# Optimization experiments

Measured on AMD Instinct MI355X. Metric: run time of the kernel, lower is better.

The kernel has to match this reference:

```python
import jax, jax.numpy as jnp
import numpy as np

WS = (7, 7)  # window size
NUM_HEADS = 16


def _relative_position_index(ws):
    # Deterministic int index table, computed exactly as in the torch module.
    coords = np.stack(np.meshgrid(np.arange(ws[0]), np.arange(ws[1]), indexing='ij'))  # [2,Wh,Ww]
    coords = coords.reshape(2, -1)                       # [2, N]
    rel = coords[:, :, None] - coords[:, None, :]        # [2, N, N]
    rel = rel.transpose(1, 2, 0)                         # [N, N, 2]
    rel = rel + np.array([ws[0] - 1, ws[1] - 1])
    rel[:, :, 0] *= 2 * ws[1] - 1
    return jnp.asarray(rel.sum(-1), dtype=jnp.int32)     # [N, N]


def setup_inputs() -> dict:
    key = jax.random.key(0)
    ks = jax.random.split(key, 5)
    B_, N, C = 2048, WS[0] * WS[1], 512
    nw = 64
    return {
        'x': jax.random.normal(ks[0], (B_, N, C), dtype=jnp.float32),
        'mask': jax.random.normal(ks[1], (nw, N, N), dtype=jnp.float32),
        'qkv_w': jax.random.normal(ks[2], (3 * C, C), dtype=jnp.float32) * 0.02,
        'qkv_b': jax.random.normal(ks[3], (3 * C,), dtype=jnp.float32) * 0.02,
        'rpb_table': jax.random.normal(ks[4], ((2 * WS[0] - 1) * (2 * WS[1] - 1), NUM_HEADS), dtype=jnp.float32) * 0.02,
    }


def reference(x, mask, qkv_w, qkv_b, rpb_table):
    B_, N, C = x.shape
    H = NUM_HEADS
    hd = C // H
    scale = hd ** -0.5

    # qkv projection: [B_, N, 3, H, hd] -> q, k, v each [B_, H, N, hd]
    qkv = (jnp.einsum('bnc,oc->bno', x, qkv_w) + qkv_b)
    qkv = qkv.reshape(B_, N, 3, H, hd).transpose(2, 0, 3, 1, 4)
    q, k, v = qkv[0], qkv[1], qkv[2]

    attn = jnp.einsum('bhnd,bhmd->bhnm', q * scale, k)  # [B_, H, N, N]

    rel_idx = _relative_position_index(WS)                       # [N, N]
    bias = rpb_table[rel_idx.reshape(-1)].reshape(N, N, H)       # gather
    attn = attn + bias.transpose(2, 0, 1)[None]                  # [1, H, N, N]

    nw = mask.shape[0]
    attn = attn.reshape(B_ // nw, nw, H, N, N) + mask[None, :, None]
    attn = attn.reshape(B_, H, N, N)
    attn = jax.nn.softmax(attn, axis=-1)

    out = jnp.einsum('bhnm,bhmd->bhnd', attn, v)
    out = out.transpose(0, 2, 1, 3).reshape(B_, N, C)
    # NOTE: source assigns `X = self.proj(x)` but returns `x`, so the
    # output projection is dead code; we faithfully return pre-proj output.
    return out
```

## Files before the change

kernel.cpp:

```cpp
#include <hip/hip_runtime.h>
#include <cstdint>
#include <cstddef>

typedef __bf16 bf16x8 __attribute__((ext_vector_type(8)));
typedef float f32x4 __attribute__((ext_vector_type(4)));
typedef unsigned short u16x8 __attribute__((ext_vector_type(8)));

#define VT_LD 56
#define LDE 144

__device__ __forceinline__ unsigned short f2bf(float f) {
  unsigned int u = __builtin_bit_cast(unsigned int, f);
  u += 0x7FFFu + ((u >> 16) & 1u);
  return (unsigned short)(u >> 16);
}

__device__ __forceinline__ void gload_lds16(const void* g, void* l) {
  __builtin_amdgcn_global_load_lds((const __attribute__((address_space(1))) void*)g,
                                   (__attribute__((address_space(3))) void*)l, 16, 0, 0);
}

__global__ void conv_f2b_k(const float* __restrict__ src, unsigned short* __restrict__ dst, long n8) {
  long i = (long)blockIdx.x * blockDim.x + threadIdx.x;
  long stride = (long)gridDim.x * blockDim.x;
  for (; i < n8; i += stride) {
    float4 a = *(const float4*)(src + i * 8);
    float4 b = *(const float4*)(src + i * 8 + 4);
    u16x8 p;
    p[0]=f2bf(a.x); p[1]=f2bf(a.y); p[2]=f2bf(a.z); p[3]=f2bf(a.w);
    p[4]=f2bf(b.x); p[5]=f2bf(b.y); p[6]=f2bf(b.z); p[7]=f2bf(b.w);
    *(u16x8*)(dst + i * 8) = p;
  }
}

__global__ void build_bias_k(const float* __restrict__ rpb, float* __restrict__ biasT) {
  int idx = blockIdx.x * 256 + threadIdx.x;
  if (idx >= 16 * 2401) return;
  int h = idx / 2401;
  int rem = idx - h * 2401;
  int i = rem / 49, j = rem - (rem / 49) * 49;
  int r1 = i / 7, c1 = i - r1 * 7;
  int r2 = j / 7, c2 = j - r2 * 7;
  int ri = (r1 - r2 + 6) * 13 + (c1 - c2 + 6);
  biasT[idx] = rpb[ri * 16 + h];
}

__global__ __launch_bounds__(256, 3) void qkv_gemm_k(
    const unsigned short* __restrict__ xb, const float* __restrict__ qkv_b,
    const unsigned short* __restrict__ wb,
    unsigned short* __restrict__ qs, unsigned short* __restrict__ kk,
    unsigned short* __restrict__ vt)
{
  __shared__ __align__(16) unsigned short smem[18432];
  unsigned short* Ab = smem;
  unsigned short* Bb = smem + 8192;

  int bid = blockIdx.x;
  int sw = (bid & 7) * 1176 + (bid >> 3);
  int mt = sw / 12, nt = sw - mt * 12;
  long m0 = (long)mt * 128;
  int  n0 = nt * 128;
  int  s  = n0 >> 9;

  int t = threadIdx.x;
  int lane = t & 63, wv = t >> 6;
  int g = lane >> 4, q = lane & 15;
  int wrow = wv >> 1, wcol = wv & 1;

  f32x4 acc[4][4] = {};

  int schunk = (t & 3) ^ ((t >> 3) & 3);
  const unsigned short* ag0 = xb + (m0 + (t >> 2)) * 512 + schunk * 8;
  const unsigned short* ag1 = ag0 + 64 * 512;
  const unsigned short* bg0 = wb + (size_t)(n0 + (t >> 2)) * 512 + schunk * 8;
  const unsigned short* bg1 = bg0 + 64 * 512;
  unsigned short* alA  = Ab + wv * 512;
  unsigned short* alA2 = Ab + 2048 + wv * 512;
  unsigned short* blB  = Bb + wv * 512;
  unsigned short* blB2 = Bb + 2048 + wv * 512;

  int roff = (8 * g) ^ (((q >> 1) & 3) << 3);
  const unsigned short* arb = Ab + (wrow * 64 + q) * 32 + roff;
  const unsigned short* brb = Bb + (wcol * 64 + q) * 32 + roff;

#define STAGE(KT, BOFF) do {                    \
    int kof = (KT) * 32;                        \
    gload_lds16(ag0 + kof, alA  + (BOFF));      \
    gload_lds16(ag1 + kof, alA2 + (BOFF));      \
    gload_lds16(bg0 + kof, blB  + (BOFF));      \
    gload_lds16(bg1 + kof, blB2 + (BOFF));      \
  } while (0)

#define COMPUTE(BOFF) do {                                                     \
    bf16x8 af[4], bfr[4];                                                      \
    _Pragma("unroll")                                                          \
    for (int i2 = 0; i2 < 4; ++i2) af[i2]  = *(const bf16x8*)(arb + (BOFF) + i2 * 512); \
    _Pragma("unroll")                                                          \
    for (int j2 = 0; j2 < 4; ++j2) bfr[j2] = *(const bf16x8*)(brb + (BOFF) + j2 * 512); \
    _Pragma("unroll")                                                          \
    for (int i2 = 0; i2 < 4; ++i2)                                             \
      _Pragma("unroll")                                                        \
      for (int j2 = 0; j2 < 4; ++j2)                                           \
        acc[i2][j2] = __builtin_amdgcn_mfma_f32_16x16x32_bf16(af[i2], bfr[j2], acc[i2][j2], 0, 0, 0); \
  } while (0)

  STAGE(0, 0);
  __syncthreads();
  for (int kt = 0; kt < 16; kt += 2) {
    STAGE(kt + 1, 4096);
    COMPUTE(0);
    __syncthreads();
    if (kt + 2 < 16) STAGE(kt + 2, 0);
    COMPUTE(4096);
    __syncthreads();
  }
#undef STAGE
#undef COMPUTE

  int   nl[4];
  float bias[4];
  #pragma unroll
  for (int j2 = 0; j2 < 4; ++j2) {
    nl[j2] = wcol * 64 + j2 * 16 + q;
    bias[j2] = qkv_b[n0 + nl[j2]];
  }

  if (s < 2) {
    float sc = (s == 0) ? 0.17677669529663687f : 1.0f;
    #pragma unroll
    for (int i2 = 0; i2 < 4; ++i2) {
      #pragma unroll
      for (int r = 0; r < 4; ++r) {
        int ml = wrow * 64 + i2 * 16 + 4 * g + r;
        #pragma unroll
        for (int j2 = 0; j2 < 4; ++j2)
          smem[ml * LDE + nl[j2]] = f2bf((acc[i2][j2][r] + bias[j2]) * sc);
      }
    }
    __syncthreads();
    unsigned short* dst = (s == 0) ? qs : kk;
    int c8 = (t & 15) * 8;
    int d0 = c8 & 31;
    int h  = ((n0 + c8) >> 5) & 15;
    #pragma unroll
    for (int p = 0; p < 8; ++p) {
      int row = p * 16 + (t >> 4);
      unsigned int gm = (unsigned int)m0 + row;
      unsigned int b  = gm / 49;
      unsigned int i  = gm - b * 49;
      u16x8 val = *(const u16x8*)(smem + row * LDE + c8);
      *(u16x8*)(dst + ((size_t)(b * 16 + h) * 49 + i) * 32 + d0) = val;
    }
  } else {
    #pragma unroll
    for (int j2 = 0; j2 < 4; ++j2) {
      int d = nl[j2] & 31;
      int h = ((n0 + nl[j2]) >> 5) & 15;
      #pragma unroll
      for (int i2 = 0; i2 < 4; ++i2) {
        unsigned int gm0 = (unsigned int)m0 + wrow * 64 + i2 * 16 + 4 * g;
        unsigned int b0 = gm0 / 49;
        unsigned int i0 = gm0 - b0 * 49;
        unsigned short hv[4];
        #pragma unroll
        for (int r = 0; r < 4; ++r) hv[r] = f2bf(acc[i2][j2][r] + bias[j2]);
        if (i0 <= 45) {
          unsigned short* base = vt + ((size_t)(b0 * 16 + h) * 32 + d) * VT_LD;
          if ((i0 & 1) == 0) {
            *(unsigned int*)(base + i0)     = (unsigned int)hv[0] | ((unsigned int)hv[1] << 16);
            *(unsigned int*)(base + i0 + 2) = (unsigned int)hv[2] | ((unsigned int)hv[3] << 16);
          } else {
            base[i0] = hv[0];
            *(unsigned int*)(base + i0 + 1) = (unsigned int)hv[1] | ((unsigned int)hv[2] << 16);
            base[i0 + 3] = hv[3];
          }
        } else {
          #pragma unroll
          for (int r = 0; r < 4; ++r) {
            unsigned int gm = gm0 + r;
            unsigned int b = gm / 49;
            unsigned int i = gm - b * 49;
            vt[((size_t)(b * 16 + h) * 32 + d) * VT_LD + i] = hv[r];
          }
        }
      }
    }
  }
}

__global__ __launch_bounds__(256, 2) void win_attn_k(
    const unsigned short* __restrict__ qs, const unsigned short* __restrict__ kk,
    const unsigned short* __restrict__ vt, const float* __restrict__ biasT,
    const float* __restrict__ mask, float* __restrict__ out)
{
  __shared__ float mlds[49 * 49];
  __shared__ unsigned short plds[4][64 * 72];

  int b = blockIdx.x;
  int t = threadIdx.x;
  int lane = t & 63, wv = t >> 6;
  int g = lane >> 4, q = lane & 15;

  const float* msrc = mask + (size_t)(b & 63) * 2401;
  for (int idx = t; idx < 2401; idx += 256) mlds[idx] = msrc[idx];
  __syncthreads();

  unsigned short* pl = plds[wv];

  for (int hh = 0; hh < 4; ++hh) {
    int h = wv * 4 + hh;
    const unsigned short* qh = qs + (size_t)(b * 16 + h) * (49 * 32);
    const unsigned short* kh = kk + (size_t)(b * 16 + h) * (49 * 32);
    const unsigned short* vh = vt + (size_t)(b * 16 + h) * (32 * VT_LD);
    const float* bhp = biasT + h * 2401;

    bf16x8 aq[4], bk[4];
    #pragma unroll
    for (int it = 0; it < 4; ++it) {
      int row = it * 16 + q; row = row > 48 ? 48 : row;
      aq[it] = *(const bf16x8*)(qh + row * 32 + 8 * g);
    }
    #pragma unroll
    for (int jt = 0; jt < 4; ++jt) {
      int row = jt * 16 + q; row = row > 48 ? 48 : row;
      bk[jt] = *(const bf16x8*)(kh + row * 32 + 8 * g);
    }
    f32x4 zero = {0.f, 0.f, 0.f, 0.f};
    f32x4 st[4][4];
    __builtin_amdgcn_s_setprio(1);
    #pragma unroll
    for (int it = 0; it < 4; ++it)
      #pragma unroll
      for (int jt = 0; jt < 4; ++jt)
        st[it][jt] = __builtin_amdgcn_mfma_f32_16x16x32_bf16(aq[it], bk[jt], zero, 0, 0, 0);
    __builtin_amdgcn_s_setprio(0);

    float rinv[4][4];
    #pragma unroll
    for (int it = 0; it < 4; ++it) {
      #pragma unroll
      for (int r = 0; r < 4; ++r) {
        int i = it * 16 + 4 * g + r;
        int ic = i > 48 ? 48 : i;
        float vj[4];
        #pragma unroll
        for (int jt = 0; jt < 4; ++jt) {
          int j = jt * 16 + q;
          float val;
          if (j < 49) val = st[it][jt][r] + bhp[ic * 49 + j] + mlds[ic * 49 + j];
          else        val = -__builtin_inff();
          vj[jt] = val;
        }
        float mx = fmaxf(fmaxf(vj[0], vj[1]), fmaxf(vj[2], vj[3]));
        #pragma unroll
        for (int off = 1; off < 16; off <<= 1) mx = fmaxf(mx, __shfl_xor(mx, off));
        float sm = 0.f;
        #pragma unroll
        for (int jt = 0; jt < 4; ++jt) {
          float p = __expf(vj[jt] - mx);
          st[it][jt][r] = p;
          sm += p;
        }
        #pragma unroll
        for (int off = 1; off < 16; off <<= 1) sm += __shfl_xor(sm, off);
        rinv[it][r] = 1.0f / sm;
      }
    }

    #pragma unroll
    for (int it = 0; it < 4; ++it)
      #pragma unroll
      for (int jt = 0; jt < 4; ++jt)
        #pragma unroll
        for (int r = 0; r < 4; ++r) {
          int i = it * 16 + 4 * g + r;
          int j = jt * 16 + q;
          pl[i * 72 + j] = f2bf(st[it][jt][r]);
        }

    f32x4 oacc[4][2] = {};
    #pragma unroll
    for (int ktt = 0; ktt < 2; ++ktt) {
      bf16x8 pa[4], bv[2];
      #pragma unroll
      for (int it = 0; it < 4; ++it)
        pa[it] = *(const bf16x8*)(pl + (it * 16 + q) * 72 + ktt * 32 + 8 * g);
      #pragma unroll
      for (int dt = 0; dt < 2; ++dt)
        bv[dt] = *(const bf16x8*)(vh + (dt * 16 + q) * VT_LD + ktt * 32 + 8 * g);
      __builtin_amdgcn_s_setprio(1);
      #pragma unroll
      for (int it = 0; it < 4; ++it)
        #pragma unroll
        for (int dt = 0; dt < 2; ++dt)
          oacc[it][dt] = __builtin_amdgcn_mfma_f32_16x16x32_bf16(pa[it], bv[dt], oacc[it][dt], 0, 0, 0);
      __builtin_amdgcn_s_setprio(0);
    }

    #pragma unroll
    for (int it = 0; it < 4; ++it) {
      #pragma unroll
      for (int dt = 0; dt < 2; ++dt) {
        #pragma unroll
        for (int r = 0; r < 4; ++r) {
          int i = it * 16 + 4 * g + r;
          if (i < 49) {
            int d = dt * 16 + q;
            out[(size_t)(b * 49 + i) * 512 + h * 32 + d] = oacc[it][dt][r] * rinv[it][r];
          }
        }
      }
    }
  }
}

extern "C" void kernel_launch(void* const* d_in, const int* in_sizes, int n_in,
                              void* d_out, int out_size, void* d_ws, size_t ws_size,
                              hipStream_t stream) {
  const float* x     = (const float*)d_in[0];
  const float* mask  = (const float*)d_in[1];
  const float* qkv_w = (const float*)d_in[2];
  const float* qkv_b = (const float*)d_in[3];
  const float* rpb   = (const float*)d_in[4];
  float* out = (float*)d_out;

  const size_t QS_OFF   = 0;
  const size_t KK_OFF   = 102760448;
  const size_t VT_OFF   = 205520896;
  const size_t BIAS_OFF = 322961408;
  const size_t WB_OFF   = 323115072;
  const size_t NEED     = 324687936;
  if (ws_size < NEED) return;

  char* ws = (char*)d_ws;
  unsigned short* qsb   = (unsigned short*)(ws + QS_OFF);
  unsigned short* kkb   = (unsigned short*)(ws + KK_OFF);
  unsigned short* vtb   = (unsigned short*)(ws + VT_OFF);
  float*          biasT = (float*)(ws + BIAS_OFF);
  unsigned short* wb    = (unsigned short*)(ws + WB_OFF);

  unsigned short* xb = (unsigned short*)d_out;

  conv_f2b_k<<<2048, 256, 0, stream>>>(x, xb, 6422528);
  conv_f2b_k<<<512, 256, 0, stream>>>(qkv_w, wb, 98304);
  build_bias_k<<<151, 256, 0, stream>>>(rpb, biasT);
  qkv_gemm_k<<<9408, 256, 0, stream>>>(xb, qkv_b, wb, qsb, kkb, vtb);
  win_attn_k<<<2048, 256, 0, stream>>>(qsb, kkb, vtb, biasT, mask, out);
}
```

Before: 503.5 us.

## Transpose attention scores, pad bias/mask rows, prefetch next head's Q/K in window attention

Swaps the MFMA operands so each lane holds four consecutive key columns of one query row. This allows vectorized bias/mask loads from padded (stride 52) tables and cuts the softmax reductions from four shuffle rounds per row to two. The bias table is stored as bf16, and normalization is folded into the P values before they are written to LDS as packed 64-bit stores. Q/K for the next head and V for the current head are loaded early to overlap global latency. The risks are higher register pressure under launch_bounds(256,2) and slightly lower bias precision from bf16.

After: 441.8 us. -12.2%, faster.

```diff
diff --git a/kernel.cpp b/kernel.cpp
--- a/kernel.cpp
+++ b/kernel.cpp
@@ -5,14 +5,23 @@
 typedef __bf16 bf16x8 __attribute__((ext_vector_type(8)));
 typedef float f32x4 __attribute__((ext_vector_type(4)));
 typedef unsigned short u16x8 __attribute__((ext_vector_type(8)));
+typedef unsigned short u16x4 __attribute__((ext_vector_type(4)));
+typedef unsigned int u32x2 __attribute__((ext_vector_type(2)));
 
 #define VT_LD 56
 #define LDE 144
+#define BSTRIDE 52
+#define BSZ 2548
+#define PLD 80
 
 __device__ __forceinline__ unsigned short f2bf(float f) {
   unsigned int u = __builtin_bit_cast(unsigned int, f);
   u += 0x7FFFu + ((u >> 16) & 1u);
   return (unsigned short)(u >> 16);
+}
+__device__ __forceinline__ float bf2f(unsigned short h) {
+  unsigned int u = (unsigned int)h << 16;
+  return __builtin_bit_cast(float, u);
 }
 
 __device__ __forceinline__ void gload_lds16(const void* g, void* l) {
@@ -33,16 +42,20 @@
   }
 }
 
-__global__ void build_bias_k(const float* __restrict__ rpb, float* __restrict__ biasT) {
+__global__ void build_bias_k(const float* __restrict__ rpb, unsigned short* __restrict__ biasT) {
   int idx = blockIdx.x * 256 + threadIdx.x;
-  if (idx >= 16 * 2401) return;
-  int h = idx / 2401;
-  int rem = idx - h * 2401;
-  int i = rem / 49, j = rem - (rem / 49) * 49;
-  int r1 = i / 7, c1 = i - r1 * 7;
-  int r2 = j / 7, c2 = j - r2 * 7;
-  int ri = (r1 - r2 + 6) * 13 + (c1 - c2 + 6);
-  biasT[idx] = rpb[ri * 16 + h];
+  if (idx >= 16 * BSZ) return;
+  int h = idx / BSZ;
+  int rem = idx - h * BSZ;
+  int i = rem / BSTRIDE, j = rem - (rem / BSTRIDE) * BSTRIDE;
+  unsigned short v = 0;
+  if (j < 49) {
+    int r1 = i / 7, c1 = i - r1 * 7;
+    int r2 = j / 7, c2 = j - r2 * 7;
+    int ri = (r1 - r2 + 6) * 13 + (c1 - c2 + 6);
+    v = f2bf(rpb[ri * 16 + h]);
+  }
+  biasT[idx] = v;
 }
 
 __global__ __launch_bounds__(256, 3) void qkv_gemm_k(
@@ -190,11 +203,11 @@
 
 __global__ __launch_bounds__(256, 2) void win_attn_k(
     const unsigned short* __restrict__ qs, const unsigned short* __restrict__ kk,
-    const unsigned short* __restrict__ vt, const float* __restrict__ biasT,
+    const unsigned short* __restrict__ vt, const unsigned short* __restrict__ biasT,
     const float* __restrict__ mask, float* __restrict__ out)
 {
-  __shared__ float mlds[49 * 49];
-  __shared__ unsigned short plds[4][64 * 72];
+  __shared__ float mlds[BSZ];
+  __shared__ unsigned short plds[4][64 * PLD];
 
   int b = blockIdx.x;
   int t = threadIdx.x;
@@ -202,29 +215,33 @@
   int g = lane >> 4, q = lane & 15;
 
   const float* msrc = mask + (size_t)(b & 63) * 2401;
-  for (int idx = t; idx < 2401; idx += 256) mlds[idx] = msrc[idx];
+  for (int idx = t; idx < BSZ; idx += 256) {
+    int i = idx / BSTRIDE, j = idx - (idx / BSTRIDE) * BSTRIDE;
+    mlds[idx] = (j < 49) ? msrc[i * 49 + j] : 0.0f;
+  }
   __syncthreads();
 
   unsigned short* pl = plds[wv];
-
+  const float NINF = -__builtin_inff();
+
+  int rc[4];
+  rc[0] = q; rc[1] = 16 + q; rc[2] = 32 + q; rc[3] = 48;
+
+  int h0 = wv * 4;
+  const unsigned short* qh = qs + (size_t)(b * 16 + h0) * (49 * 32);
+  const unsigned short* kh = kk + (size_t)(b * 16 + h0) * (49 * 32);
+  bf16x8 ak[4], bq[4];
+  #pragma unroll
+  for (int jt = 0; jt < 4; ++jt) ak[jt] = *(const bf16x8*)(kh + rc[jt] * 32 + 8 * g);
+  #pragma unroll
+  for (int it = 0; it < 4; ++it) bq[it] = *(const bf16x8*)(qh + rc[it] * 32 + 8 * g);
+
+  #pragma unroll
   for (int hh = 0; hh < 4; ++hh) {
     int h = wv * 4 + hh;
-    const unsigned short* qh = qs + (size_t)(b * 16 + h) * (49 * 32);
-    const unsigned short* kh = kk + (size_t)(b * 16 + h) * (49 * 32);
-    const unsigned short* vh = vt + (size_t)(b * 16 + h) * (32 * VT_LD);
-    const float* bhp = biasT + h * 2401;
-
-    bf16x8 aq[4], bk[4];
-    #pragma unroll
-    for (int it = 0; it < 4; ++it) {
-      int row = it * 16 + q; row = row > 48 ? 48 : row;
-      aq[it] = *(const bf16x8*)(qh + row * 32 + 8 * g);
-    }
-    #pragma unroll
-    for (int jt = 0; jt < 4; ++jt) {
-      int row = jt * 16 + q; row = row > 48 ? 48 : row;
-      bk[jt] = *(const bf16x8*)(kh + row * 32 + 8 * g);
-    }
+    const unsigned short* vh  = vt + (size_t)(b * 16 + h) * (32 * VT_LD);
+    const unsigned short* bh2 = biasT + h * BSZ;
+
     f32x4 zero = {0.f, 0.f, 0.f, 0.f};
     f32x4 st[4][4];
     __builtin_amdgcn_s_setprio(1);
@@ -232,68 +249,89 @@
     for (int it = 0; it < 4; ++it)
       #pragma unroll
       for (int jt = 0; jt < 4; ++jt)
-        st[it][jt] = __builtin_amdgcn_mfma_f32_16x16x32_bf16(aq[it], bk[jt], zero, 0, 0, 0);
+        st[it][jt] = __builtin_amdgcn_mfma_f32_16x16x32_bf16(ak[jt], bq[it], zero, 0, 0, 0);
     __builtin_amdgcn_s_setprio(0);
 
-    float rinv[4][4];
+    bf16x8 akn[4], bqn[4];
+    if (hh < 3) {
+      const unsigned short* qh2 = qh + 49 * 32;
+      const unsigned short* kh2 = kh + 49 * 32;
+      #pragma unroll
+      for (int jt = 0; jt < 4; ++jt) akn[jt] = *(const bf16x8*)(kh2 + rc[jt] * 32 + 8 * g);
+      #pragma unroll
+      for (int it = 0; it < 4; ++it) bqn[it] = *(const bf16x8*)(qh2 + rc[it] * 32 + 8 * g);
+      qh = qh2; kh = kh2;
+    }
+    bf16x8 bv[2][2];
+    #pragma unroll
+    for (int ktt = 0; ktt < 2; ++ktt)
+      #pragma unroll
+      for (int dt = 0; dt < 2; ++dt)
+        bv[ktt][dt] = *(const bf16x8*)(vh + (dt * 16 + q) * VT_LD + ktt * 32 + 8 * g);
+
     #pragma unroll
     for (int it = 0; it < 4; ++it) {
-      #pragma unroll
-      for (int r = 0; r < 4; ++r) {
-        int i = it * 16 + 4 * g + r;
-        int ic = i > 48 ? 48 : i;
-        float vj[4];
-        #pragma unroll
-        for (int jt = 0; jt < 4; ++jt) {
-          int j = jt * 16 + q;
-          float val;
-          if (j < 49) val = st[it][jt][r] + bhp[ic * 49 + j] + mlds[ic * 49 + j];
-          else        val = -__builtin_inff();
-          vj[jt] = val;
+      int i = it * 16 + q;
+      int ic = i > 48 ? 48 : i;
+      f32x4 pv4[4];
+      f32x4 vm = {NINF, NINF, NINF, NINF};
+      #pragma unroll
+      for (int jt = 0; jt < 4; ++jt) {
+        if (jt == 3 && g > 0) {
+          pv4[3] = (f32x4){NINF, NINF, NINF, NINF};
+        } else {
+          u16x4 bu = *(const u16x4*)(bh2 + ic * BSTRIDE + jt * 16 + 4 * g);
+          f32x4 m4 = *(const f32x4*)(mlds + ic * BSTRIDE + jt * 16 + 4 * g);
+          f32x4 sv = st[it][jt];
+          #pragma unroll
+          for (int r = 0; r < 4; ++r) sv[r] += bf2f(bu[r]) + m4[r];
+          if (jt == 3) {
+            sv[1] = NINF; sv[2] = NINF; sv[3] = NINF;
+          }
+          pv4[jt] = sv;
+          #pragma unroll
+          for (int r = 0; r < 4; ++r) vm[r] = fmaxf(vm[r], sv[r]);
         }
-        float mx = fmaxf(fmaxf(vj[0], vj[1]), fmaxf(vj[2], vj[3]));
-        #pragma unroll
-        for (int off = 1; off < 16; off <<= 1) mx = fmaxf(mx, __shfl_xor(mx, off));
-        float sm = 0.f;
-        #pragma unroll
-        for (int jt = 0; jt < 4; ++jt) {
-          float p = __expf(vj[jt] - mx);
-          st[it][jt][r] = p;
-          sm += p;
+      }
+      float mx = fmaxf(fmaxf(vm[0], vm[1]), fmaxf(vm[2], vm[3]));
+      mx = fmaxf(mx, __shfl_xor(mx, 16));
+      mx = fmaxf(mx, __shfl_xor(mx, 32));
+      f32x4 vs = zero;
+      #pragma unroll
+      for (int jt = 0; jt < 4; ++jt) {
+        #pragma unroll
+        for (int r = 0; r < 4; ++r) {
+          float p = __expf(pv4[jt][r] - mx);
+          pv4[jt][r] = p;
+          vs[r] += p;
         }
-        #pragma unroll
-        for (int off = 1; off < 16; off <<= 1) sm += __shfl_xor(sm, off);
-        rinv[it][r] = 1.0f / sm;
-      }
-    }
-
-    #pragma unroll
-    for (int it = 0; it < 4; ++it)
-      #pragma unroll
-      for (int jt = 0; jt < 4; ++jt)
-        #pragma unroll
-        for (int r = 0; r < 4; ++r) {
-          int i = it * 16 + 4 * g + r;
-          int j = jt * 16 + q;
-          pl[i * 72 + j] = f2bf(st[it][jt][r]);
-        }
+      }
+      float sm = (vs[0] + vs[1]) + (vs[2] + vs[3]);
+      sm += __shfl_xor(sm, 16);
+      sm += __shfl_xor(sm, 32);
+      float rv = 1.0f / sm;
+      #pragma unroll
+      for (int jt = 0; jt < 4; ++jt) {
+        unsigned int lo = (unsigned int)f2bf(pv4[jt][0] * rv) | ((unsigned int)f2bf(pv4[jt][1] * rv) << 16);
+        unsigned int hi = (unsigned int)f2bf(pv4[jt][2] * rv) | ((unsigned int)f2bf(pv4[jt][3] * rv) << 16);
+        u32x2 w = {lo, hi};
+        *(u32x2*)(pl + i * PLD + jt * 16 + 4 * g) = w;
+      }
+    }
 
     f32x4 oacc[4][2] = {};
     #pragma unroll
     for (int ktt = 0; ktt < 2; ++ktt) {
-      bf16x8 pa[4], bv[2];
+      bf16x8 pa[4];
       #pragma unroll
       for (int it = 0; it < 4; ++it)
-        pa[it] = *(const bf16x8*)(pl + (it * 16 + q) * 72 + ktt * 32 + 8 * g);
-      #pragma unroll
-      for (int dt = 0; dt < 2; ++dt)
-        bv[dt] = *(const bf16x8*)(vh + (dt * 16 + q) * VT_LD + ktt * 32 + 8 * g);
+        pa[it] = *(const bf16x8*)(pl + (it * 16 + q) * PLD + ktt * 32 + 8 * g);
       __builtin_amdgcn_s_setprio(1);
       #pragma unroll
       for (int it = 0; it < 4; ++it)
         #pragma unroll
         for (int dt = 0; dt < 2; ++dt)
-          oacc[it][dt] = __builtin_amdgcn_mfma_f32_16x16x32_bf16(pa[it], bv[dt], oacc[it][dt], 0, 0, 0);
+          oacc[it][dt] = __builtin_amdgcn_mfma_f32_16x16x32_bf16(pa[it], bv[ktt][dt], oacc[it][dt], 0, 0, 0);
       __builtin_amdgcn_s_setprio(0);
     }
 
@@ -306,10 +344,17 @@
           int i = it * 16 + 4 * g + r;
           if (i < 49) {
             int d = dt * 16 + q;
-            out[(size_t)(b * 49 + i) * 512 + h * 32 + d] = oacc[it][dt][r] * rinv[it][r];
+            out[(size_t)(b * 49 + i) * 512 + h * 32 + d] = oacc[it][dt][r];
           }
         }
       }
+    }
+
+    if (hh < 3) {
+      #pragma unroll
+      for (int jt = 0; jt < 4; ++jt) ak[jt] = akn[jt];
+      #pragma unroll
+      for (int it = 0; it < 4; ++it) bq[it] = bqn[it];
     }
   }
 }
@@ -328,22 +373,22 @@
   const size_t KK_OFF   = 102760448;
   const size_t VT_OFF   = 205520896;
   const size_t BIAS_OFF = 322961408;
-  const size_t WB_OFF   = 323115072;
-  const size_t NEED     = 324687936;
+  const size_t WB_OFF   = 323042944;
+  const size_t NEED     = 324615808;
   if (ws_size < NEED) return;
 
   char* ws = (char*)d_ws;
   unsigned short* qsb   = (unsigned short*)(ws + QS_OFF);
   unsigned short* kkb   = (unsigned short*)(ws + KK_OFF);
   unsigned short* vtb   = (unsigned short*)(ws + VT_OFF);
-  float*          biasT = (float*)(ws + BIAS_OFF);
+  unsigned short* biasT = (unsigned short*)(ws + BIAS_OFF);
   unsigned short* wb    = (unsigned short*)(ws + WB_OFF);
 
   unsigned short* xb = (unsigned short*)d_out;
 
   conv_f2b_k<<<2048, 256, 0, stream>>>(x, xb, 6422528);
   conv_f2b_k<<<512, 256, 0, stream>>>(qkv_w, wb, 98304);
-  build_bias_k<<<151, 256, 0, stream>>>(rpb, biasT);
+  build_bias_k<<<160, 256, 0, stream>>>(rpb, biasT);
   qkv_gemm_k<<<9408, 256, 0, stream>>>(xb, qkv_b, wb, qsb, kkb, vtb);
   win_attn_k<<<2048, 256, 0, stream>>>(qsb, kkb, vtb, biasT, mask, out);
 }
```
